# Optimization experiments

Hardware: AMD Instinct MI355X
Metric: run time of the kernel (lower is better)

Reference implementation:

```python
import jax, jax.numpy as jnp
import numpy as np

B, IN_DIM, HID, SUB_IN, SUB_OUT, GRID = 4096, 256, 512, 256, 256, 32
LN_EPS = 1e-5


def setup_inputs() -> dict:
    key = jax.random.key(0)
    ks = jax.random.split(key, 16)
    inp = {
        'x':  jax.random.normal(ks[0], (B, IN_DIM), jnp.float32),
        'h0': jax.random.normal(ks[1], (B, HID), jnp.float32),
        'c0': jax.random.normal(ks[2], (B, HID), jnp.float32),
        's0': jax.random.normal(ks[3], (B, SUB_OUT), jnp.float32),
        # LSTM gate params
        'kernel':  jax.random.normal(ks[4], (IN_DIM, 3 * HID), jnp.float32) * 0.05,
        'rkernel': jax.random.normal(ks[5], (HID, 3 * HID), jnp.float32) * 0.05,
        'bias':    jnp.zeros((3 * HID,), jnp.float32),
        # sub-layer recurrent mixing kernels (num_sub_layers=1)
        'sub_kx': jax.random.normal(ks[6], (1, IN_DIM, SUB_IN), jnp.float32) * 0.05,
        'sub_kh': jax.random.normal(ks[7], (1, SUB_OUT, SUB_IN), jnp.float32) * 0.05,
        'sub_tkan_kernel': jax.random.normal(ks[8], (1, 2 * SUB_OUT), jnp.float32) * 0.05,
        # Fourier KAN coefficients: (2, outdim, indim, gridsize) + bias
        'fc': jax.random.normal(ks[9], (2, SUB_OUT, SUB_IN, GRID), jnp.float32) / np.sqrt(SUB_IN * GRID),
        'fb': jnp.zeros((SUB_OUT,), jnp.float32),
        # aggregation + layer norm
        'agg_w': jax.random.normal(ks[10], (SUB_OUT, HID), jnp.float32) * 0.05,
        'agg_b': jnp.zeros((HID,), jnp.float32),
        'ln_g':  jnp.ones((HID,), jnp.float32),
        'ln_b':  jnp.zeros((HID,), jnp.float32),
    }
    return inp


def _fourier_kan(z, fc, fb):
    # z: [B, SUB_IN] -> [B, SUB_OUT]
    k = jnp.arange(1, GRID + 1, dtype=z.dtype)          # [G]
    ang = z[:, :, None] * k                             # [B, IN, G]
    return (jnp.einsum('big,oig->bo', jnp.cos(ang), fc[0])
            + jnp.einsum('big,oig->bo', jnp.sin(ang), fc[1]) + fb)


def reference(x, h0, c0, s0, kernel, rkernel, bias, sub_kx, sub_kh,
              sub_tkan_kernel, fc, fb, agg_w, agg_b, ln_g, ln_b):
    # LSTM-style gates (note: candidate also passes through sigmoid then tanh,
    # exactly as in the torch source)
    gates = jax.nn.sigmoid(x @ kernel + h0 @ rkernel + bias)      # [B, 3H]
    i, f, c_cand = jnp.split(gates, 3, axis=-1)
    c = f * c0 + i * jnp.tanh(c_cand)                             # [B, H]

    # single KAN sub-layer
    agg_in = x @ sub_kx[0] + s0 @ sub_kh[0]                       # [B, SUB_IN]
    sub_out = _fourier_kan(agg_in, fc, fb)                        # [B, SUB_OUT]
    rk_h, rk_x = jnp.split(sub_tkan_kernel[0], 2)                 # [SUB_OUT] each
    new_s = rk_h * sub_out + s0 * rk_x

    # aggregation -> output gate
    o = jax.nn.sigmoid(sub_out @ agg_w + agg_b)                   # [B, H]
    h = o * jnp.tanh(c)

    # layer norm
    mu = jnp.mean(h, axis=-1, keepdims=True)
    var = jnp.mean(jnp.square(h - mu), axis=-1, keepdims=True)
    h = (h - mu) * jax.lax.rsqrt(var + LN_EPS) * ln_g + ln_b
    return (h, c, new_s)
```

## Files before the change

### kernel.cpp

```cpp
#include <hip/hip_runtime.h>
#include <hip/hip_bf16.h>

typedef __bf16 bf16_t;
typedef __bf16 bf16x2 __attribute__((ext_vector_type(2)));
typedef __bf16 bf16x4 __attribute__((ext_vector_type(4)));
typedef __bf16 bf16x8 __attribute__((ext_vector_type(8)));
typedef float  f32x4  __attribute__((ext_vector_type(4)));

#define NB 4096
#define IN_DIM 256
#define HID 512
#define SUB 256
#define GRID_ 32

__device__ __forceinline__ float fract_f(float x) {
#if __has_builtin(__builtin_amdgcn_fractf)
  return __builtin_amdgcn_fractf(x);
#else
  return x - floorf(x);
#endif
}
__device__ __forceinline__ float cos_rev(float rev) {
#if __has_builtin(__builtin_amdgcn_cosf)
  return __builtin_amdgcn_cosf(rev);
#else
  return __cosf(rev * 6.283185307179586f);
#endif
}
__device__ __forceinline__ float sin_rev(float rev) {
#if __has_builtin(__builtin_amdgcn_sinf)
  return __builtin_amdgcn_sinf(rev);
#else
  return __sinf(rev * 6.283185307179586f);
#endif
}
__device__ __forceinline__ float sigm(float v) { return 1.f / (1.f + __expf(-v)); }
__device__ __forceinline__ float fast_tanh(float x) {
  float e = __expf(2.f * x);
  return (e - 1.f) / (e + 1.f);
}
#define INV2PI 0.15915494309189535f

#define O_XHI   0ull
#define O_XLO   2097152ull
#define O_H0    4194304ull
#define O_S0H   8388608ull
#define O_S0L   10485760ull
#define O_FCB   12582912ull
#define O_O     12582912ull
#define O_KT    20971520ull
#define O_RKT   21757952ull
#define O_AWT   23330816ull
#define O_KXH   23592960ull
#define O_KXL   23724032ull
#define O_KHH   23855104ull
#define O_KHL   23986176ull
#define O_TC    24117248ull
#define O_SOB   32505856ull
#define O_AGG   34603008ull
#define O_P3    38797312ull

__device__ __forceinline__ void tconv_body(const float* __restrict__ src,
                                           bf16_t* __restrict__ hi,
                                           bf16_t* __restrict__ lo,
                                           int R, int C, int bx, int by,
                                           bool wantlo, float scale) {
  __shared__ float t[32][33];
  int c0 = bx * 32, r0 = by * 32;
  int tx = threadIdx.x & 31, ty = threadIdx.x >> 5;
#pragma unroll
  for (int rr = 0; rr < 4; rr++) {
    int r = ty + rr * 8;
    t[r][tx] = src[(size_t)(r0 + r) * C + c0 + tx];
  }
  __syncthreads();
#pragma unroll
  for (int rr = 0; rr < 4; rr++) {
    int cl = ty + rr * 8;
    float f = t[tx][cl] * scale;
    bf16_t h = (bf16_t)f;
    size_t oi = (size_t)(c0 + cl) * R + r0 + tx;
    hi[oi] = h;
    if (wantlo) lo[oi] = (bf16_t)(f - (float)h);
  }
}

__global__ __launch_bounds__(256) void k_prep(const float* __restrict__ x,
                                              const float* __restrict__ h0,
                                              const float* __restrict__ s0,
                                              const float* __restrict__ fc,
                                              const float* __restrict__ Wk,
                                              const float* __restrict__ Wr,
                                              const float* __restrict__ aw,
                                              const float* __restrict__ kx,
                                              const float* __restrict__ kh,
                                              bf16_t* __restrict__ xhi, bf16_t* __restrict__ xlo,
                                              bf16_t* __restrict__ h0b,
                                              bf16_t* __restrict__ s0h, bf16_t* __restrict__ s0l,
                                              bf16_t* __restrict__ fcb2,
                                              bf16_t* __restrict__ kt,
                                              bf16_t* __restrict__ rkt,
                                              bf16_t* __restrict__ awt,
                                              bf16_t* __restrict__ kxh, bf16_t* __restrict__ kxl,
                                              bf16_t* __restrict__ khh, bf16_t* __restrict__ khl) {
  int bid = blockIdx.x;
  if (bid < 2048) {
    for (int q = bid * 256 + threadIdx.x; q < 2097152; q += 524288) {
      if (q < 1048576) {
        const float* src; bf16_t* hi; bf16_t* lo = nullptr; int base;
        if (q < 262144)       { src = x;  hi = xhi; lo = xlo; base = q; }
        else if (q < 786432)  { src = h0; hi = h0b;           base = q - 262144; }
        else                  { src = s0; hi = s0h; lo = s0l; base = q - 786432; }
        float4 v = *(const float4*)(src + (size_t)base * 4);
        bf16x4 h; h[0] = (bf16_t)v.x; h[1] = (bf16_t)v.y; h[2] = (bf16_t)v.z; h[3] = (bf16_t)v.w;
        *(bf16x4*)(hi + (size_t)base * 4) = h;
        if (lo) {
          bf16x4 l;
          l[0] = (bf16_t)(v.x - (float)h[0]); l[1] = (bf16_t)(v.y - (float)h[1]);
          l[2] = (bf16_t)(v.z - (float)h[2]); l[3] = (bf16_t)(v.w - (float)h[3]);
          *(bf16x4*)(lo + (size_t)base * 4) = l;
        }
      } else {
        int f = q - 1048576;
        int e = f * 4;
        int g = e & 31, i = (e >> 5) & 255, o = (e >> 13) & 255, s = e >> 21;
        float4 v = *(const float4*)(fc + (size_t)e);
        bf16x4 h; h[0] = (bf16_t)v.x; h[1] = (bf16_t)v.y; h[2] = (bf16_t)v.z; h[3] = (bf16_t)v.w;
        int nb = o >> 7, wn = (o >> 6) & 1, j = (o >> 4) & 3, lr = o & 15;
        int g4 = g >> 3, t0 = g & 7;
        size_t idx = ((((((size_t)(i * 2 + nb) * 2 + wn) * 4 + j) * 2 + s) * 4 + g4) * 16 + lr) * 8 + t0;
        *(bf16x4*)(fcb2 + idx) = h;
      }
    }
  } else {
    int b = bid - 2048;
    if (b < 384)       { tconv_body(Wk, kt,  nullptr, 256, 1536, b % 48, b / 48, false, 1.f); }
    else if (b < 1152) { b -= 384;  tconv_body(Wr, rkt, nullptr, 512, 1536, b % 48, b / 48, false, 1.f); }
    else if (b < 1280) { b -= 1152; tconv_body(aw, awt, nullptr, 256, 512,  b % 16, b / 16, false, 1.f); }
    else if (b < 1344) { b -= 1280; tconv_body(kx, kxh, kxl,     256, 256,  b % 8,  b / 8,  true, INV2PI); }
    else               { b -= 1344; tconv_body(kh, khh, khl,     256, 256,  b % 8,  b / 8,  true, INV2PI); }
  }
}

struct Pass { const bf16_t* A; const bf16_t* Bt; int K; int lda; int ldbt; };
struct GArgs {
  Pass p[6]; int np;
  const float* bias;
  int act;
  float* out; bf16_t* outb; int ldout;
};

template<int BM, int BN>
__global__ __launch_bounds__(512) void k_gemm(GArgs g) {
  constexpr int MI = BM / 32;
  constexpr int NJ = BN / 64;
  constexpr int IA = (BM * 8) / 512;
  constexpr int IB = (BN * 8) / 512;
  __shared__ bf16_t smA[BM * 64];
  __shared__ bf16_t smB[BN * 64];
  const int tid = threadIdx.x;
  const int m0 = blockIdx.y * BM, n0 = blockIdx.x * BN;
  const int wv = tid >> 6, lane = tid & 63;
  const int wm = wv >> 2, wn = wv & 3;
  const int lr = lane & 15, g4 = lane >> 4;

  f32x4 acc[MI][NJ];
#pragma unroll
  for (int i = 0; i < MI; i++)
#pragma unroll
    for (int j = 0; j < NJ; j++) acc[i][j] = f32x4{0.f, 0.f, 0.f, 0.f};

  for (int ps = 0; ps < g.np; ps++) {
    const bf16_t* A = g.p[ps].A;
    const bf16_t* Bt = g.p[ps].Bt;
    const int K = g.p[ps].K, lda = g.p[ps].lda, ldbt = g.p[ps].ldbt;
    for (int k0 = 0; k0 < K; k0 += 64) {
      bf16x8 ar[IA], br[IB];
#pragma unroll
      for (int r = 0; r < IA; r++) {
        int task = tid + r * 512, row = task >> 3, t = task & 7, sf = t ^ (row & 7);
        ar[r] = *(const bf16x8*)(A + (size_t)(m0 + row) * lda + k0 + sf * 8);
      }
#pragma unroll
      for (int r = 0; r < IB; r++) {
        int task = tid + r * 512, row = task >> 3, t = task & 7, sf = t ^ (row & 7);
        br[r] = *(const bf16x8*)(Bt + (size_t)(n0 + row) * ldbt + k0 + sf * 8);
      }
      __syncthreads();
#pragma unroll
      for (int r = 0; r < IA; r++) {
        int task = tid + r * 512, row = task >> 3, t = task & 7;
        *(bf16x8*)(smA + row * 64 + t * 8) = ar[r];
      }
#pragma unroll
      for (int r = 0; r < IB; r++) {
        int task = tid + r * 512, row = task >> 3, t = task & 7;
        *(bf16x8*)(smB + row * 64 + t * 8) = br[r];
      }
      __syncthreads();
#pragma unroll
      for (int ks = 0; ks < 2; ks++) {
        bf16x8 af[MI], bfr[NJ];
#pragma unroll
        for (int i = 0; i < MI; i++) {
          int row = wm * (BM / 2) + i * 16 + lr;
          af[i] = *(const bf16x8*)(smA + row * 64 + ((ks * 4 + g4) ^ (lr & 7)) * 8);
        }
#pragma unroll
        for (int j = 0; j < NJ; j++) {
          int row = wn * (BN / 4) + j * 16 + lr;
          bfr[j] = *(const bf16x8*)(smB + row * 64 + ((ks * 4 + g4) ^ (lr & 7)) * 8);
        }
#pragma unroll
        for (int i = 0; i < MI; i++)
#pragma unroll
          for (int j = 0; j < NJ; j++)
            acc[i][j] = __builtin_amdgcn_mfma_f32_16x16x32_bf16(af[i], bfr[j], acc[i][j], 0, 0, 0);
      }
    }
  }
#pragma unroll
  for (int i = 0; i < MI; i++)
#pragma unroll
    for (int j = 0; j < NJ; j++) {
      int col = n0 + wn * (BN / 4) + j * 16 + lr;
      float bb = g.bias ? g.bias[col] : 0.f;
#pragma unroll
      for (int r = 0; r < 4; r++) {
        int row = m0 + wm * (BM / 2) + i * 16 + (lane >> 4) * 4 + r;
        float v = acc[i][j][r] + bb;
        if (g.act == 1) v = sigm(v);
        if (g.outb) g.outb[(size_t)row * g.ldout + col] = (bf16_t)v;
        else        g.out [(size_t)row * g.ldout + col] = v;
      }
    }
}

struct GatesArgs {
  const bf16_t* xhi; const bf16_t* h0b; const bf16_t* kt; const bf16_t* rkt;
  const float* bias; const float* c0; float* c_out; bf16_t* tc;
};

__global__ __launch_bounds__(256, 2) void k_gates(GatesArgs ga) {
  __shared__ bf16_t smA[64 * 64];
  __shared__ bf16_t smB[3 * 64 * 64];
  const int tid = threadIdx.x;
  const int n0 = blockIdx.x * 64;
  const int m0 = blockIdx.y * 64;
  const int wv = tid >> 6, lane = tid & 63;
  const int wm = wv >> 1, wn = wv & 1;
  const int lr = lane & 15, g4 = lane >> 4;

  f32x4 acc[3][2][2];
#pragma unroll
  for (int t = 0; t < 3; t++)
#pragma unroll
    for (int i = 0; i < 2; i++)
#pragma unroll
      for (int j = 0; j < 2; j++) acc[t][i][j] = f32x4{0.f, 0.f, 0.f, 0.f};

  for (int ps = 0; ps < 2; ps++) {
    const bf16_t* A  = ps ? ga.h0b : ga.xhi;
    const bf16_t* Bt = ps ? ga.rkt : ga.kt;
    const int K = ps ? 512 : 256, ld = K;
    for (int k0 = 0; k0 < K; k0 += 64) {
      bf16x8 ar[2], br[6];
#pragma unroll
      for (int r = 0; r < 2; r++) {
        int task = tid + r * 256, row = task >> 3, t = task & 7, sf = t ^ (row & 7);
        ar[r] = *(const bf16x8*)(A + (size_t)(m0 + row) * ld + k0 + sf * 8);
      }
#pragma unroll
      for (int r = 0; r < 6; r++) {
        int task = tid + r * 256;
        int gate = task >> 9, rem = task & 511, o = rem >> 3, t = rem & 7, sf = t ^ (o & 7);
        br[r] = *(const bf16x8*)(Bt + (size_t)(gate * 512 + n0 + o) * ld + k0 + sf * 8);
      }
      __syncthreads();
#pragma unroll
      for (int r = 0; r < 2; r++) {
        int task = tid + r * 256, row = task >> 3, t = task & 7;
        *(bf16x8*)(smA + row * 64 + t * 8) = ar[r];
      }
#pragma unroll
      for (int r = 0; r < 6; r++) {
        int task = tid + r * 256;
        int gate = task >> 9, rem = task & 511, o = rem >> 3, t = rem & 7;
        *(bf16x8*)(smB + (gate * 64 + o) * 64 + t * 8) = br[r];
      }
      __syncthreads();
#pragma unroll
      for (int ks = 0; ks < 2; ks++) {
        bf16x8 af[2];
#pragma unroll
        for (int i = 0; i < 2; i++) {
          int row = wm * 32 + i * 16 + lr;
          af[i] = *(const bf16x8*)(smA + row * 64 + ((ks * 4 + g4) ^ (lr & 7)) * 8);
        }
#pragma unroll
        for (int t = 0; t < 3; t++) {
          bf16x8 bfr[2];
#pragma unroll
          for (int j = 0; j < 2; j++) {
            int row = wn * 32 + j * 16 + lr;
            bfr[j] = *(const bf16x8*)(smB + (t * 64 + row) * 64 + ((ks * 4 + g4) ^ (lr & 7)) * 8);
          }
#pragma unroll
          for (int i = 0; i < 2; i++)
#pragma unroll
            for (int j = 0; j < 2; j++)
              acc[t][i][j] = __builtin_amdgcn_mfma_f32_16x16x32_bf16(af[i], bfr[j], acc[t][i][j], 0, 0, 0);
        }
      }
    }
  }
#pragma unroll
  for (int i = 0; i < 2; i++)
#pragma unroll
    for (int j = 0; j < 2; j++) {
      int col = n0 + wn * 32 + j * 16 + lr;
      float bi = ga.bias[col], bf_ = ga.bias[512 + col], bc = ga.bias[1024 + col];
#pragma unroll
      for (int r = 0; r < 4; r++) {
        int row = m0 + wm * 32 + i * 16 + g4 * 4 + r;
        size_t idx = (size_t)row * 512 + col;
        float iv = sigm(acc[0][i][j][r] + bi);
        float fv = sigm(acc[1][i][j][r] + bf_);
        float cc = sigm(acc[2][i][j][r] + bc);
        float cv = fv * ga.c0[idx] + iv * fast_tanh(cc);
        ga.c_out[idx] = cv;
        ga.tc[idx] = (bf16_t)fast_tanh(cv);
      }
    }
}

struct FArgs { const float* agg; const bf16_t* fcb2; float* P[8]; };

__global__ __launch_bounds__(128, 2) void k_fourier(FArgs fa) {
  __shared__ float  zl[64 * 33];
  __shared__ bf16_t Asm[2][64 * 64];
  const int tid = threadIdx.x;
  const int bx = blockIdx.x;
  const int q = bx & 7, nb = (bx >> 3) & 1, mb = bx >> 4;
  const int m0 = mb * 64, n0 = nb * 128, i0 = q * 32;
  const int wv = tid >> 6, lane = tid & 63;
  const int wn = wv;
  const int lr = lane & 15, g4 = lane >> 4;

#pragma unroll
  for (int r = 0; r < 4; r++) {
    int task = tid + r * 128, row = task >> 3, seg = task & 7;
    float4 v = *(const float4*)(fa.agg + (size_t)(m0 + row) * 256 + i0 + seg * 4);
    zl[row * 33 + seg * 4 + 0] = v.x;
    zl[row * 33 + seg * 4 + 1] = v.y;
    zl[row * 33 + seg * 4 + 2] = v.z;
    zl[row * 33 + seg * 4 + 3] = v.w;
  }

  const bf16_t* pB = fa.fcb2 + (size_t)i0 * 16384 + nb * 8192 + wn * 4096 + lane * 8;
  auto loadB = [&](int i, bf16x8 (&b)[8]) {
#pragma unroll
    for (int ks = 0; ks < 2; ks++)
#pragma unroll
      for (int j = 0; j < 4; j++)
        b[ks * 4 + j] = *(const bf16x8*)(pB + (size_t)i * 16384 + j * 1024 + ks * 512);
  };

  const int grow = tid >> 1, hp = tid & 1;
  const float* zp = zl + grow * 33;
  const int as0 = grow * 64 + (((2 * hp    ) ^ (grow & 7)) * 8);
  const int as1 = grow * 64 + (((2 * hp + 1) ^ (grow & 7)) * 8);
  const int as2 = grow * 64 + (((4 + 2 * hp) ^ (grow & 7)) * 8);
  const int as3 = grow * 64 + (((5 + 2 * hp) ^ (grow & 7)) * 8);
  auto genA = [&](int i, bf16_t* Ab) {
    float zr = zp[i];
    bf16x8 c0v, c1v, s0v, s1v;
#pragma unroll
    for (int t = 0; t < 8; t++) {
      float r0 = fract_f(zr * (float)(hp * 16 + t + 1));
      float r1 = fract_f(zr * (float)(hp * 16 + 8 + t + 1));
      c0v[t] = (bf16_t)cos_rev(r0); s0v[t] = (bf16_t)sin_rev(r0);
      c1v[t] = (bf16_t)cos_rev(r1); s1v[t] = (bf16_t)sin_rev(r1);
    }
    *(bf16x8*)(Ab + as0) = c0v;
    *(bf16x8*)(Ab + as1) = c1v;
    *(bf16x8*)(Ab + as2) = s0v;
    *(bf16x8*)(Ab + as3) = s1v;
  };

  int offA[8];
#pragma unroll
  for (int ks = 0; ks < 2; ks++)
#pragma unroll
    for (int i4 = 0; i4 < 4; i4++)
      offA[ks * 4 + i4] = (i4 * 16 + lr) * 64 + ((ks * 4 + g4) ^ (lr & 7)) * 8;

  f32x4 acc[4][4];
#pragma unroll
  for (int i = 0; i < 4; i++)
#pragma unroll
    for (int j = 0; j < 4; j++) acc[i][j] = f32x4{0.f, 0.f, 0.f, 0.f};

  auto domfma = [&](const bf16x8 (&af)[8], const bf16x8 (&b)[8]) {
    __builtin_amdgcn_s_setprio(1);
#pragma unroll
    for (int ks = 0; ks < 2; ks++)
#pragma unroll
      for (int i4 = 0; i4 < 4; i4++)
#pragma unroll
        for (int j = 0; j < 4; j++)
          acc[i4][j] = __builtin_amdgcn_mfma_f32_16x16x32_bf16(af[ks * 4 + i4], b[ks * 4 + j], acc[i4][j], 0, 0, 0);
    __builtin_amdgcn_s_setprio(0);
  };
  auto readA = [&](const bf16_t* Ac, bf16x8 (&af)[8]) {
#pragma unroll
    for (int t = 0; t < 8; t++) af[t] = *(const bf16x8*)(Ac + offA[t]);
  };

  bf16x8 bA_[8], bB_[8];
  __syncthreads();
  loadB(0, bA_);
  genA(0, Asm[0]);
  asm volatile("s_waitcnt lgkmcnt(0)" ::: "memory");
  __builtin_amdgcn_s_barrier();

#pragma unroll 1
  for (int it = 0; it < 16; it++) {
    const int i = it * 2;
    bf16x8 af[8];
    if (i < 31) loadB(i + 1, bB_);
    readA(Asm[0], af);
    if (i < 31) genA(i + 1, Asm[1]);
    domfma(af, bA_);
    asm volatile("s_waitcnt lgkmcnt(0)" ::: "memory");
    __builtin_amdgcn_s_barrier();
    if (i + 2 < 32) loadB(i + 2, bA_);
    readA(Asm[1], af);
    if (i + 2 < 32) genA(i + 2, Asm[0]);
    domfma(af, bB_);
    asm volatile("s_waitcnt lgkmcnt(0)" ::: "memory");
    __builtin_amdgcn_s_barrier();
  }

  float* outp = fa.P[q];
#pragma unroll
  for (int i = 0; i < 4; i++)
#pragma unroll
    for (int j = 0; j < 4; j++) {
      int col = n0 + wn * 64 + j * 16 + lr;
#pragma unroll
      for (int r = 0; r < 4; r++) {
        int row = m0 + i * 16 + g4 * 4 + r;
        outp[(size_t)row * 256 + col] = acc[i][j][r];
      }
    }
}

struct RArgs {
  const float* P[8];
  const float* fb; const float* tk; const float* s0;
  float* news; bf16_t* sob;
};

__global__ __launch_bounds__(256) void k_freduce(RArgs ra) {
  int stride = gridDim.x * blockDim.x;
  for (int qd = blockIdx.x * blockDim.x + threadIdx.x; qd < 262144; qd += stride) {
    int i = qd * 4, o = i & 255;
    float4 v = *(const float4*)(ra.P[0] + i);
#pragma unroll
    for (int c = 1; c < 8; c++) {
      float4 p = *(const float4*)(ra.P[c] + i);
      v.x += p.x; v.y += p.y; v.z += p.z; v.w += p.w;
    }
    v.x += ra.fb[o + 0]; v.y += ra.fb[o + 1]; v.z += ra.fb[o + 2]; v.w += ra.fb[o + 3];
    bf16x4 sb; sb[0] = (bf16_t)v.x; sb[1] = (bf16_t)v.y; sb[2] = (bf16_t)v.z; sb[3] = (bf16_t)v.w;
    *(bf16x4*)(ra.sob + i) = sb;
    float4 s = *(const float4*)(ra.s0 + i);
    float4 ns;
    ns.x = ra.tk[o + 0] * v.x + ra.tk[256 + o + 0] * s.x;
    ns.y = ra.tk[o + 1] * v.y + ra.tk[256 + o + 1] * s.y;
    ns.z = ra.tk[o + 2] * v.z + ra.tk[256 + o + 2] * s.z;
    ns.w = ra.tk[o + 3] * v.w + ra.tk[256 + o + 3] * s.w;
    *(float4*)(ra.news + i) = ns;
  }
}

__global__ __launch_bounds__(256) void k_ln(const bf16_t* __restrict__ o,
                                            const bf16_t* __restrict__ tc,
                                            const float* __restrict__ lg,
                                            const float* __restrict__ lb,
                                            float* __restrict__ h) {
  int b = blockIdx.x, tid = threadIdx.x;
  bf16x2 ov = *(const bf16x2*)(o + (size_t)b * 512 + tid * 2);
  bf16x2 tv = *(const bf16x2*)(tc + (size_t)b * 512 + tid * 2);
  float h0 = (float)ov[0] * (float)tv[0], h1 = (float)ov[1] * (float)tv[1];
  float s = h0 + h1, ss = h0 * h0 + h1 * h1;
#pragma unroll
  for (int off = 32; off; off >>= 1) {
    s += __shfl_xor(s, off);
    ss += __shfl_xor(ss, off);
  }
  __shared__ float red[8];
  int wid = tid >> 6;
  if ((tid & 63) == 0) { red[wid] = s; red[4 + wid] = ss; }
  __syncthreads();
  s = red[0] + red[1] + red[2] + red[3];
  ss = red[4] + red[5] + red[6] + red[7];
  float mu = s * (1.f / 512.f);
  float var = ss * (1.f / 512.f) - mu * mu;
  float rs = rsqrtf(var + 1e-5f);
  int j = tid * 2;
  h[(size_t)b * 512 + j]     = (h0 - mu) * rs * lg[j]     + lb[j];
  h[(size_t)b * 512 + j + 1] = (h1 - mu) * rs * lg[j + 1] + lb[j + 1];
}

extern "C" void kernel_launch(void* const* d_in, const int* in_sizes, int n_in,
                              void* d_out, int out_size, void* d_ws, size_t ws_size,
                              hipStream_t stream) {
  const float* x    = (const float*)d_in[0];
  const float* h0   = (const float*)d_in[1];
  const float* c0   = (const float*)d_in[2];
  const float* s0   = (const float*)d_in[3];
  const float* Wk   = (const float*)d_in[4];
  const float* Wr   = (const float*)d_in[5];
  const float* bias = (const float*)d_in[6];
  const float* kx   = (const float*)d_in[7];
  const float* kh   = (const float*)d_in[8];
  const float* tk   = (const float*)d_in[9];
  const float* fc   = (const float*)d_in[10];
  const float* fb   = (const float*)d_in[11];
  const float* aw   = (const float*)d_in[12];
  const float* ab   = (const float*)d_in[13];
  const float* lg   = (const float*)d_in[14];
  const float* lbp  = (const float*)d_in[15];
  float* out = (float*)d_out;
  char* ws = (char*)d_ws;
  auto BF = [&](unsigned long long off) { return (bf16_t*)(ws + off); };
  auto FP = [&](unsigned long long off) { return (float*)(ws + off); };

  k_prep<<<3456, 256, 0, stream>>>(x, h0, s0, fc, Wk, Wr, aw, kx, kh,
                                   BF(O_XHI), BF(O_XLO), BF(O_H0),
                                   BF(O_S0H), BF(O_S0L), BF(O_FCB),
                                   BF(O_KT), BF(O_RKT), BF(O_AWT),
                                   BF(O_KXH), BF(O_KXL), BF(O_KHH), BF(O_KHL));

  {
    GatesArgs ga{ BF(O_XHI), BF(O_H0), BF(O_KT), BF(O_RKT), bias, c0,
                  out + 2097152, BF(O_TC) };
    k_gates<<<dim3(8, 64), 256, 0, stream>>>(ga);
  }

  {
    GArgs g{};
    g.p[0] = { BF(O_XHI), BF(O_KXH), 256, 256, 256 };
    g.p[1] = { BF(O_XHI), BF(O_KXL), 256, 256, 256 };
    g.p[2] = { BF(O_XLO), BF(O_KXH), 256, 256, 256 };
    g.p[3] = { BF(O_S0H), BF(O_KHH), 256, 256, 256 };
    g.p[4] = { BF(O_S0H), BF(O_KHL), 256, 256, 256 };
    g.p[5] = { BF(O_S0L), BF(O_KHH), 256, 256, 256 };
    g.np = 6; g.bias = nullptr; g.act = 0;
    g.out = FP(O_AGG); g.outb = nullptr; g.ldout = 256;
    k_gemm<64, 64><<<dim3(4, 64), 512, 0, stream>>>(g);
  }

  FArgs fa;
  fa.agg = FP(O_AGG); fa.fcb2 = BF(O_FCB);
  fa.P[0] = FP(0ull);
  fa.P[1] = FP(4194304ull);
  fa.P[2] = FP(8388608ull);
  for (int c = 3; c < 8; c++) fa.P[c] = FP(O_P3 + (unsigned long long)(c - 3) * 4194304ull);
  k_fourier<<<1024, 128, 0, stream>>>(fa);

  RArgs ra;
  for (int c = 0; c < 8; c++) ra.P[c] = fa.P[c];
  ra.fb = fb; ra.tk = tk; ra.s0 = s0;
  ra.news = out + 4194304; ra.sob = BF(O_SOB);
  k_freduce<<<1024, 256, 0, stream>>>(ra);

  {
    GArgs g{};
    g.p[0] = { BF(O_SOB), BF(O_AWT), 256, 256, 256 };
    g.np = 1; g.bias = ab; g.act = 1;
    g.out = nullptr; g.outb = BF(O_O); g.ldout = 512;
    k_gemm<64, 128><<<dim3(4, 64), 512, 0, stream>>>(g);
  }
  k_ln<<<4096, 256, 0, stream>>>(BF(O_O), BF(O_TC), lg, lbp, out);
}
```

Measured before the change: 113.7 us.

## Merge gates and agg GEMMs into one launch and store Fourier partials in bf16

The LSTM gate GEMM and the six-pass agg-input GEMM now run as one kernel: block index picks the branch, 512 gate blocks and 256 agg blocks. This removes one launch and lets the smaller agg GEMM fill the GPU alongside the gate blocks. The eight Fourier KAN partial-sum buffers are written in bf16 instead of fp32 and widened back to fp32 in the reduce kernel, halving that round-trip traffic. The cost is extra rounding on each partial before the sum, which also feeds the fp32 new_s output.

```diff
diff --git a/kernel.cpp b/kernel.cpp
--- a/kernel.cpp
+++ b/kernel.cpp
@@ -236,105 +236,169 @@
     }
 }
 
-struct GatesArgs {
+struct GAArgs {
   const bf16_t* xhi; const bf16_t* h0b; const bf16_t* kt; const bf16_t* rkt;
   const float* bias; const float* c0; float* c_out; bf16_t* tc;
+  const bf16_t* aggA[6]; const bf16_t* aggB[6];
+  float* agg;
 };
 
-__global__ __launch_bounds__(256, 2) void k_gates(GatesArgs ga) {
+__global__ __launch_bounds__(256, 2) void k_gatesagg(GAArgs ga) {
   __shared__ bf16_t smA[64 * 64];
   __shared__ bf16_t smB[3 * 64 * 64];
   const int tid = threadIdx.x;
-  const int n0 = blockIdx.x * 64;
-  const int m0 = blockIdx.y * 64;
   const int wv = tid >> 6, lane = tid & 63;
   const int wm = wv >> 1, wn = wv & 1;
   const int lr = lane & 15, g4 = lane >> 4;
 
-  f32x4 acc[3][2][2];
-#pragma unroll
-  for (int t = 0; t < 3; t++)
+  if (blockIdx.x < 512) {
+    const int b = blockIdx.x;
+    const int n0 = (b & 7) * 64, m0 = (b >> 3) * 64;
+    f32x4 acc[3][2][2];
+#pragma unroll
+    for (int t = 0; t < 3; t++)
+#pragma unroll
+      for (int i = 0; i < 2; i++)
+#pragma unroll
+        for (int j = 0; j < 2; j++) acc[t][i][j] = f32x4{0.f, 0.f, 0.f, 0.f};
+
+    for (int ps = 0; ps < 2; ps++) {
+      const bf16_t* A  = ps ? ga.h0b : ga.xhi;
+      const bf16_t* Bt = ps ? ga.rkt : ga.kt;
+      const int K = ps ? 512 : 256, ld = K;
+      for (int k0 = 0; k0 < K; k0 += 64) {
+        bf16x8 ar[2], br[6];
+#pragma unroll
+        for (int r = 0; r < 2; r++) {
+          int task = tid + r * 256, row = task >> 3, t = task & 7, sf = t ^ (row & 7);
+          ar[r] = *(const bf16x8*)(A + (size_t)(m0 + row) * ld + k0 + sf * 8);
+        }
+#pragma unroll
+        for (int r = 0; r < 6; r++) {
+          int task = tid + r * 256;
+          int gate = task >> 9, rem = task & 511, o = rem >> 3, t = rem & 7, sf = t ^ (o & 7);
+          br[r] = *(const bf16x8*)(Bt + (size_t)(gate * 512 + n0 + o) * ld + k0 + sf * 8);
+        }
+        __syncthreads();
+#pragma unroll
+        for (int r = 0; r < 2; r++) {
+          int task = tid + r * 256, row = task >> 3, t = task & 7;
+          *(bf16x8*)(smA + row * 64 + t * 8) = ar[r];
+        }
+#pragma unroll
+        for (int r = 0; r < 6; r++) {
+          int task = tid + r * 256;
+          int gate = task >> 9, rem = task & 511, o = rem >> 3, t = rem & 7;
+          *(bf16x8*)(smB + (gate * 64 + o) * 64 + t * 8) = br[r];
+        }
+        __syncthreads();
+#pragma unroll
+        for (int ks = 0; ks < 2; ks++) {
+          bf16x8 af[2];
+#pragma unroll
+          for (int i = 0; i < 2; i++) {
+            int row = wm * 32 + i * 16 + lr;
+            af[i] = *(const bf16x8*)(smA + row * 64 + ((ks * 4 + g4) ^ (lr & 7)) * 8);
+          }
+#pragma unroll
+          for (int t = 0; t < 3; t++) {
+            bf16x8 bfr[2];
+#pragma unroll
+            for (int j = 0; j < 2; j++) {
+              int row = wn * 32 + j * 16 + lr;
+              bfr[j] = *(const bf16x8*)(smB + (t * 64 + row) * 64 + ((ks * 4 + g4) ^ (lr & 7)) * 8);
+            }
+#pragma unroll
+            for (int i = 0; i < 2; i++)
+#pragma unroll
+              for (int j = 0; j < 2; j++)
+                acc[t][i][j] = __builtin_amdgcn_mfma_f32_16x16x32_bf16(af[i], bfr[j], acc[t][i][j], 0, 0, 0);
+          }
+        }
+      }
+    }
 #pragma unroll
     for (int i = 0; i < 2; i++)
 #pragma unroll
-      for (int j = 0; j < 2; j++) acc[t][i][j] = f32x4{0.f, 0.f, 0.f, 0.f};
-
-  for (int ps = 0; ps < 2; ps++) {
-    const bf16_t* A  = ps ? ga.h0b : ga.xhi;
-    const bf16_t* Bt = ps ? ga.rkt : ga.kt;
-    const int K = ps ? 512 : 256, ld = K;
-    for (int k0 = 0; k0 < K; k0 += 64) {
-      bf16x8 ar[2], br[6];
-#pragma unroll
-      for (int r = 0; r < 2; r++) {
-        int task = tid + r * 256, row = task >> 3, t = task & 7, sf = t ^ (row & 7);
-        ar[r] = *(const bf16x8*)(A + (size_t)(m0 + row) * ld + k0 + sf * 8);
-      }
-#pragma unroll
-      for (int r = 0; r < 6; r++) {
-        int task = tid + r * 256;
-        int gate = task >> 9, rem = task & 511, o = rem >> 3, t = rem & 7, sf = t ^ (o & 7);
-        br[r] = *(const bf16x8*)(Bt + (size_t)(gate * 512 + n0 + o) * ld + k0 + sf * 8);
-      }
-      __syncthreads();
-#pragma unroll
-      for (int r = 0; r < 2; r++) {
-        int task = tid + r * 256, row = task >> 3, t = task & 7;
-        *(bf16x8*)(smA + row * 64 + t * 8) = ar[r];
-      }
-#pragma unroll
-      for (int r = 0; r < 6; r++) {
-        int task = tid + r * 256;
-        int gate = task >> 9, rem = task & 511, o = rem >> 3, t = rem & 7;
-        *(bf16x8*)(smB + (gate * 64 + o) * 64 + t * 8) = br[r];
-      }
-      __syncthreads();
-#pragma unroll
-      for (int ks = 0; ks < 2; ks++) {
-        bf16x8 af[2];
-#pragma unroll
-        for (int i = 0; i < 2; i++) {
-          int row = wm * 32 + i * 16 + lr;
-          af[i] = *(const bf16x8*)(smA + row * 64 + ((ks * 4 + g4) ^ (lr & 7)) * 8);
-        }
-#pragma unroll
-        for (int t = 0; t < 3; t++) {
-          bf16x8 bfr[2];
+      for (int j = 0; j < 2; j++) {
+        int col = n0 + wn * 32 + j * 16 + lr;
+        float bi = ga.bias[col], bf_ = ga.bias[512 + col], bc = ga.bias[1024 + col];
+#pragma unroll
+        for (int r = 0; r < 4; r++) {
+          int row = m0 + wm * 32 + i * 16 + g4 * 4 + r;
+          size_t idx = (size_t)row * 512 + col;
+          float iv = sigm(acc[0][i][j][r] + bi);
+          float fv = sigm(acc[1][i][j][r] + bf_);
+          float cc = sigm(acc[2][i][j][r] + bc);
+          float cv = fv * ga.c0[idx] + iv * fast_tanh(cc);
+          ga.c_out[idx] = cv;
+          ga.tc[idx] = (bf16_t)fast_tanh(cv);
+        }
+      }
+  } else {
+    const int b = blockIdx.x - 512;
+    const int n0 = (b & 3) * 64, m0 = (b >> 2) * 64;
+    f32x4 acc[2][2];
+#pragma unroll
+    for (int i = 0; i < 2; i++)
+#pragma unroll
+      for (int j = 0; j < 2; j++) acc[i][j] = f32x4{0.f, 0.f, 0.f, 0.f};
+
+    for (int ps = 0; ps < 6; ps++) {
+      const bf16_t* A  = ga.aggA[ps];
+      const bf16_t* Bt = ga.aggB[ps];
+      for (int k0 = 0; k0 < 256; k0 += 64) {
+        bf16x8 ar[2], br[2];
+#pragma unroll
+        for (int r = 0; r < 2; r++) {
+          int task = tid + r * 256, row = task >> 3, t = task & 7, sf = t ^ (row & 7);
+          ar[r] = *(const bf16x8*)(A  + (size_t)(m0 + row) * 256 + k0 + sf * 8);
+          br[r] = *(const bf16x8*)(Bt + (size_t)(n0 + row) * 256 + k0 + sf * 8);
+        }
+        __syncthreads();
+#pragma unroll
+        for (int r = 0; r < 2; r++) {
+          int task = tid + r * 256, row = task >> 3, t = task & 7;
+          *(bf16x8*)(smA + row * 64 + t * 8) = ar[r];
+          *(bf16x8*)(smB + row * 64 + t * 8) = br[r];
+        }
+        __syncthreads();
+#pragma unroll
+        for (int ks = 0; ks < 2; ks++) {
+          bf16x8 af[2], bfr[2];
+#pragma unroll
+          for (int i = 0; i < 2; i++) {
+            int row = wm * 32 + i * 16 + lr;
+            af[i] = *(const bf16x8*)(smA + row * 64 + ((ks * 4 + g4) ^ (lr & 7)) * 8);
+          }
 #pragma unroll
           for (int j = 0; j < 2; j++) {
             int row = wn * 32 + j * 16 + lr;
-            bfr[j] = *(const bf16x8*)(smB + (t * 64 + row) * 64 + ((ks * 4 + g4) ^ (lr & 7)) * 8);
+            bfr[j] = *(const bf16x8*)(smB + row * 64 + ((ks * 4 + g4) ^ (lr & 7)) * 8);
           }
 #pragma unroll
           for (int i = 0; i < 2; i++)
 #pragma unroll
             for (int j = 0; j < 2; j++)
-              acc[t][i][j] = __builtin_amdgcn_mfma_f32_16x16x32_bf16(af[i], bfr[j], acc[t][i][j], 0, 0, 0);
-        }
-      }
-    }
-  }
-#pragma unroll
-  for (int i = 0; i < 2; i++)
-#pragma unroll
-    for (int j = 0; j < 2; j++) {
-      int col = n0 + wn * 32 + j * 16 + lr;
-      float bi = ga.bias[col], bf_ = ga.bias[512 + col], bc = ga.bias[1024 + col];
-#pragma unroll
-      for (int r = 0; r < 4; r++) {
-        int row = m0 + wm * 32 + i * 16 + g4 * 4 + r;
-        size_t idx = (size_t)row * 512 + col;
-        float iv = sigm(acc[0][i][j][r] + bi);
-        float fv = sigm(acc[1][i][j][r] + bf_);
-        float cc = sigm(acc[2][i][j][r] + bc);
-        float cv = fv * ga.c0[idx] + iv * fast_tanh(cc);
-        ga.c_out[idx] = cv;
-        ga.tc[idx] = (bf16_t)fast_tanh(cv);
-      }
-    }
-}
-
-struct FArgs { const float* agg; const bf16_t* fcb2; float* P[8]; };
+              acc[i][j] = __builtin_amdgcn_mfma_f32_16x16x32_bf16(af[i], bfr[j], acc[i][j], 0, 0, 0);
+        }
+      }
+    }
+#pragma unroll
+    for (int i = 0; i < 2; i++)
+#pragma unroll
+      for (int j = 0; j < 2; j++) {
+        int col = n0 + wn * 32 + j * 16 + lr;
+#pragma unroll
+        for (int r = 0; r < 4; r++) {
+          int row = m0 + wm * 32 + i * 16 + g4 * 4 + r;
+          ga.agg[(size_t)row * 256 + col] = acc[i][j][r];
+        }
+      }
+  }
+}
+
+struct FArgs { const float* agg; const bf16_t* fcb2; bf16_t* P[8]; };
 
 __global__ __launch_bounds__(128, 2) void k_fourier(FArgs fa) {
   __shared__ float  zl[64 * 33];
@@ -442,7 +506,7 @@
     __builtin_amdgcn_s_barrier();
   }
 
-  float* outp = fa.P[q];
+  bf16_t* outp = fa.P[q];
 #pragma unroll
   for (int i = 0; i < 4; i++)
 #pragma unroll
@@ -451,13 +515,13 @@
 #pragma unroll
       for (int r = 0; r < 4; r++) {
         int row = m0 + i * 16 + g4 * 4 + r;
-        outp[(size_t)row * 256 + col] = acc[i][j][r];
+        outp[(size_t)row * 256 + col] = (bf16_t)acc[i][j][r];
       }
     }
 }
 
 struct RArgs {
-  const float* P[8];
+  const bf16_t* P[8];
   const float* fb; const float* tk; const float* s0;
   float* news; bf16_t* sob;
 };
@@ -466,11 +530,11 @@
   int stride = gridDim.x * blockDim.x;
   for (int qd = blockIdx.x * blockDim.x + threadIdx.x; qd < 262144; qd += stride) {
     int i = qd * 4, o = i & 255;
-    float4 v = *(const float4*)(ra.P[0] + i);
-#pragma unroll
-    for (int c = 1; c < 8; c++) {
-      float4 p = *(const float4*)(ra.P[c] + i);
-      v.x += p.x; v.y += p.y; v.z += p.z; v.w += p.w;
+    float4 v = {0.f, 0.f, 0.f, 0.f};
+#pragma unroll
+    for (int c = 0; c < 8; c++) {
+      bf16x4 p = *(const bf16x4*)(ra.P[c] + i);
+      v.x += (float)p[0]; v.y += (float)p[1]; v.z += (float)p[2]; v.w += (float)p[3];
     }
     v.x += ra.fb[o + 0]; v.y += ra.fb[o + 1]; v.z += ra.fb[o + 2]; v.w += ra.fb[o + 3];
     bf16x4 sb; sb[0] = (bf16_t)v.x; sb[1] = (bf16_t)v.y; sb[2] = (bf16_t)v.z; sb[3] = (bf16_t)v.w;
@@ -545,30 +609,24 @@
                                    BF(O_KXH), BF(O_KXL), BF(O_KHH), BF(O_KHL));
 
   {
-    GatesArgs ga{ BF(O_XHI), BF(O_H0), BF(O_KT), BF(O_RKT), bias, c0,
-                  out + 2097152, BF(O_TC) };
-    k_gates<<<dim3(8, 64), 256, 0, stream>>>(ga);
-  }
-
-  {
-    GArgs g{};
-    g.p[0] = { BF(O_XHI), BF(O_KXH), 256, 256, 256 };
-    g.p[1] = { BF(O_XHI), BF(O_KXL), 256, 256, 256 };
-    g.p[2] = { BF(O_XLO), BF(O_KXH), 256, 256, 256 };
-    g.p[3] = { BF(O_S0H), BF(O_KHH), 256, 256, 256 };
-    g.p[4] = { BF(O_S0H), BF(O_KHL), 256, 256, 256 };
-    g.p[5] = { BF(O_S0L), BF(O_KHH), 256, 256, 256 };
-    g.np = 6; g.bias = nullptr; g.act = 0;
-    g.out = FP(O_AGG); g.outb = nullptr; g.ldout = 256;
-    k_gemm<64, 64><<<dim3(4, 64), 512, 0, stream>>>(g);
+    GAArgs ga{};
+    ga.xhi = BF(O_XHI); ga.h0b = BF(O_H0); ga.kt = BF(O_KT); ga.rkt = BF(O_RKT);
+    ga.bias = bias; ga.c0 = c0; ga.c_out = out + 2097152; ga.tc = BF(O_TC);
+    ga.aggA[0] = BF(O_XHI); ga.aggB[0] = BF(O_KXH);
+    ga.aggA[1] = BF(O_XHI); ga.aggB[1] = BF(O_KXL);
+    ga.aggA[2] = BF(O_XLO); ga.aggB[2] = BF(O_KXH);
+    ga.aggA[3] = BF(O_S0H); ga.aggB[3] = BF(O_KHH);
+    ga.aggA[4] = BF(O_S0H); ga.aggB[4] = BF(O_KHL);
+    ga.aggA[5] = BF(O_S0L); ga.aggB[5] = BF(O_KHH);
+    ga.agg = FP(O_AGG);
+    k_gatesagg<<<768, 256, 0, stream>>>(ga);
   }
 
   FArgs fa;
   fa.agg = FP(O_AGG); fa.fcb2 = BF(O_FCB);
-  fa.P[0] = FP(0ull);
-  fa.P[1] = FP(4194304ull);
-  fa.P[2] = FP(8388608ull);
-  for (int c = 3; c < 8; c++) fa.P[c] = FP(O_P3 + (unsigned long long)(c - 3) * 4194304ull);
+  for (int c = 0; c < 6; c++) fa.P[c] = BF((unsigned long long)c * 2097152ull);
+  fa.P[6] = BF(O_P3);
+  fa.P[7] = BF(O_P3 + 2097152ull);
   k_fourier<<<1024, 128, 0, stream>>>(fa);
 
   RArgs ra;
```

After: 96.40 us. 15.2% less time.
